# Kernel tuning notes

Hardware: AMD Instinct MI355X
Metric: run time of the kernel (lower is better)

Reference implementation:

```python
import jax, jax.numpy as jnp
import numpy as np
from jax import lax

CW = 8       # current_window
PW = 8       # pretrain_window
HEADS = 8
LOG100 = float(np.log(100.0))


def setup_inputs() -> dict:
    key = jax.random.key(0)
    ks = jax.random.split(key, 8)
    B, H, W, C = 8, 126, 126, 256
    f32 = jnp.float32
    return {
        "x": jax.random.normal(ks[0], (B, H, W, C), f32),
        "w_qkv": jax.random.normal(ks[1], (C, 3 * C), f32) * 0.02,      # 1x1 conv, no bias
        "w_dw": jax.random.normal(ks[2], (3, 3, 1, 3 * C), f32) * 0.1,  # depthwise 3x3, HWIO
        "ln_gamma": jnp.ones((3 * C,), f32),
        "ln_beta": jnp.zeros((3 * C,), f32),
        "q_bias": jnp.zeros((C,), f32),
        "v_bias": jnp.zeros((C,), f32),
        "scale": jnp.full((HEADS, 1, 1), np.log(10.0), f32),
        "cpb_w0": jax.random.normal(ks[3], (2, 512), f32) * 0.02,
        "cpb_b0": jnp.zeros((512,), f32),
        "cpb_w1": jax.random.normal(ks[4], (512, HEADS), f32) * 0.02,   # no bias, sigmoid
        "w_proj": jax.random.normal(ks[5], (C, C), f32) * 0.02,
    }


def _l2n(t):
    # tf.math.l2_normalize with epsilon=1.55e-5
    return t * lax.rsqrt(jnp.maximum(jnp.sum(t * t, axis=-1, keepdims=True), 1.55e-5))


def _cpb_bias(cpb_w0, cpb_b0, cpb_w1, cw, L, heads):
    # log-spaced continuous relative position table (static)
    rel = np.arange(1 - cw, cw, dtype=np.float32)
    rel = np.stack(np.meshgrid(rel, rel, indexing='ij'), axis=-1)  # [2cw-1, 2cw-1, 2]
    rel = rel * (8.0 / (PW - 1.0))
    rel = np.sign(rel) * np.log1p(np.abs(rel)) / np.log(8.0)
    ri = np.arange(cw)
    ri = np.stack(np.meshgrid(ri, ri, indexing='ij'), axis=0).reshape(2, -1)
    ri = ri[:, :, None] - ri[:, None, :] + (cw - 1)
    relidx = (ri[0] * (2 * cw - 1) + ri[1]).reshape(-1)  # [L*L]
    h = jax.nn.relu(jnp.asarray(rel.reshape(-1, 2)) @ cpb_w0 + cpb_b0)
    bias = jax.nn.sigmoid(h @ cpb_w1) * 16.0             # [(2cw-1)^2, heads]
    bias = bias[jnp.asarray(relidx)].reshape(L, L, heads)
    return bias.transpose(2, 0, 1)                        # [heads, L, L]


def reference(x, w_qkv, w_dw, ln_gamma, ln_beta, q_bias, v_bias, scale,
              cpb_w0, cpb_b0, cpb_w1, w_proj):
    B, H, W, C = x.shape
    cw, heads = CW, HEADS
    hd = C // heads
    L = cw * cw

    # qkv 1x1 conv + depthwise 3x3 + layernorm (ConvNorm)
    qkv = jnp.einsum('bhwc,cd->bhwd', x, w_qkv)           # [B,H,W,3C]
    qkv = lax.conv_general_dilated(qkv, w_dw, (1, 1), 'SAME',
                                   dimension_numbers=('NHWC', 'HWIO', 'NHWC'),
                                   feature_group_count=3 * C)
    mu = jnp.mean(qkv, axis=-1, keepdims=True)
    var = jnp.mean(jnp.square(qkv - mu), axis=-1, keepdims=True)
    qkv = (qkv - mu) * lax.rsqrt(var + 1e-5) * ln_gamma + ln_beta
    qkv = qkv + jnp.concatenate([q_bias, jnp.zeros_like(q_bias), v_bias])

    # pad to multiple of window, grid-partition (MaxViT-style strided grid)
    pad_h, pad_w = (-H) % cw, (-W) % cw
    hb, wb = pad_h // 2, pad_w // 2
    qkv = jnp.pad(qkv, ((0, 0), (hb, pad_h - hb), (wb, pad_w - wb), (0, 0)))
    Hp, Wp = H + pad_h, W + pad_w
    Hb, Wb = Hp // cw, Wp // cw
    nw = Hb * Wb
    qkv = qkv.reshape(B, cw, Hb, cw, Wb, 3, heads, hd)
    qkv = qkv.transpose(0, 2, 4, 6, 1, 3, 5, 7).reshape(B * nw, heads, L, 3, hd)
    q, k, v = qkv[..., 0, :], qkv[..., 1, :], qkv[..., 2, :]

    # cosine attention with learned per-head log-scale (clamped at log 100)
    q, k = _l2n(q), _l2n(k)
    ls = jnp.exp(jnp.minimum(scale, LOG100))              # [heads,1,1]
    attn = jnp.einsum('nhqd,nhkd->nhqk', q * ls, k)

    attn = attn + _cpb_bias(cpb_w0, cpb_b0, cpb_w1, cw, L, heads)[None]

    if pad_h + pad_w > 0:
        m = jnp.pad(jnp.ones((1, H, W, 1), attn.dtype),
                    ((0, 0), (hb, pad_h - hb), (wb, pad_w - wb), (0, 0)))
        m = m.reshape(1, cw, Hb, cw, Wb, 1).transpose(0, 2, 4, 1, 3, 5).reshape(nw, L)
        mbias = -100.0 * (m == 0).astype(attn.dtype)       # [nw, L] over keys
        attn = attn.reshape(B, nw, heads, L, L) + mbias[None, :, None, None, :]
        attn = attn.reshape(B * nw, heads, L, L)

    attn = jax.nn.softmax(attn, axis=-1)
    out = jnp.einsum('nhqk,nhkd->nhqd', attn, v)           # [B*nw, heads, L, hd]

    # reverse grid partition + crop + projection
    out = out.reshape(B, Hb, Wb, heads, cw, cw, hd)
    out = out.transpose(0, 4, 1, 5, 2, 3, 6).reshape(B, Hp, Wp, C)
    out = out[:, hb:hb + H, wb:wb + W]
    return jnp.einsum('bhwc,cd->bhwd', out, w_proj)
```

## Files before the change

### kernel.cpp

```cpp
#include <hip/hip_runtime.h>

typedef unsigned short ushort;
typedef __bf16 bf16x8 __attribute__((ext_vector_type(8)));
typedef float f32x4 __attribute__((ext_vector_type(4)));
typedef float f4 __attribute__((ext_vector_type(4)));
typedef unsigned short us8 __attribute__((ext_vector_type(8)));
typedef unsigned short us4 __attribute__((ext_vector_type(4)));
typedef unsigned u32x4v __attribute__((ext_vector_type(4)));

#define NPIX 127008
#define HDIM 126
#define WDIM 126

__device__ __forceinline__ float bf2f(ushort u) {
  unsigned v = ((unsigned)u) << 16;
  return __builtin_bit_cast(float, v);
}
__device__ __forceinline__ ushort f2bf(float f) {
  unsigned x = __builtin_bit_cast(unsigned, f);
  x += 0x7fffu + ((x >> 16) & 1u);
  return (ushort)(x >> 16);
}

__global__ void k_cvt_x(const float* __restrict__ x, ushort* __restrict__ xb, int n8) {
  const int stride = gridDim.x * blockDim.x;
  for (int i = blockIdx.x * blockDim.x + threadIdx.x; i < n8; i += stride) {
    const f4 a = *(const f4*)&x[(size_t)i * 8];
    const f4 b = *(const f4*)&x[(size_t)i * 8 + 4];
    us8 o;
#pragma unroll
    for (int j = 0; j < 4; ++j) { o[j] = f2bf(a[j]); o[4 + j] = f2bf(b[j]); }
    *(us8*)&xb[(size_t)i * 8] = o;
  }
}

__global__ void k_cvt_wT(const float* __restrict__ in, ushort* __restrict__ out, int N, int K) {
  const int t = blockIdx.x * 256 + threadIdx.x;
  const int n = t / K, k = t - n * K;
  out[t] = f2bf(in[(size_t)k * N + n]);
}

__device__ __forceinline__ float frel(int i) {
  const float v = (float)(i - 7) * (8.0f / 7.0f);
  const float a = log1pf(fabsf(v)) * 0.4808983469629878f;
  return v < 0.f ? -a : a;
}

__global__ __launch_bounds__(256) void k_cpb1(const float* __restrict__ w0,
    const float* __restrict__ b0, const float* __restrict__ w1, float* __restrict__ tmp) {
  const int p = blockIdx.x * 4 + (threadIdx.x >> 6);
  const int lane = threadIdx.x & 63;
  if (p >= 225) return;
  const float r0 = frel(p / 15), r1 = frel(p % 15);
  float hv[8];
#pragma unroll
  for (int jj = 0; jj < 8; ++jj) {
    const int j = lane * 8 + jj;
    hv[jj] = fmaxf(0.f, r0 * w0[j] + r1 * w0[512 + j] + b0[j]);
  }
  for (int h = 0; h < 8; ++h) {
    float part = 0.f;
#pragma unroll
    for (int jj = 0; jj < 8; ++jj) part += hv[jj] * w1[(lane * 8 + jj) * 8 + h];
    for (int o = 32; o; o >>= 1) part += __shfl_xor(part, o);
    if (lane == 0) tmp[p * 8 + h] = 16.f / (1.f + __expf(-part));
  }
}

__global__ void k_cpb2(const float* __restrict__ tmp, float* __restrict__ biasV) {
  const int t = blockIdx.x * 256 + threadIdx.x;
  const int h = t >> 12, rest = t & 4095;
  const int ki = rest >> 10, g = (rest >> 8) & 3, q = (rest >> 2) & 63, r = rest & 3;
  const int key = ki * 16 + g * 4 + r;
  const int d0 = (q >> 3) - (key >> 3) + 7, d1 = (q & 7) - (key & 7) + 7;
  biasV[t] = tmp[(d0 * 15 + d1) * 8 + h];
}

#define GLL(g, l) __builtin_amdgcn_global_load_lds( \
    (const __attribute__((address_space(1))) void*)(g), \
    (__attribute__((address_space(3))) void*)(l), 16, 0, 0)

template <int OUTF, int NX>
__global__ __launch_bounds__(256) void k_gemm(const ushort* __restrict__ A,
                                              const ushort* __restrict__ Bt,
                                              void* __restrict__ Cv, int M, int N) {
  constexpr int K = 256;
  __shared__ ushort lsA[128 * 32];
  __shared__ ushort lsB[128 * 32];
  const int tid = threadIdx.x;
  const int wid = tid >> 6, lane = tid & 63;

  const int nwg = gridDim.x;
  const int q8 = nwg >> 3, r8 = nwg & 7;
  const int xcd = blockIdx.x & 7, pos = blockIdx.x >> 3;
  const int lin = (xcd < r8) ? xcd * (q8 + 1) + pos
                             : r8 * (q8 + 1) + (xcd - r8) * q8 + pos;
  const int m0 = (lin / NX) * 128, n0 = (lin % NX) * 128;

  f32x4 acc[4][4];
#pragma unroll
  for (int i = 0; i < 4; ++i)
#pragma unroll
    for (int j = 0; j < 4; ++j) acc[i][j] = 0.f;

  const int srow = tid >> 2, sk = (tid & 3) * 8;
  const int aw = (wid >> 1) * 64, bw = (wid & 1) * 64;
  const int fr = lane & 15, kg = (lane >> 4) * 8;
  char* lA = (char*)lsA + wid * 1024;
  char* lB = (char*)lsB + wid * 1024;

  int ra0 = m0 + srow;      if (ra0 >= M) ra0 = M - 1;
  int ra1 = m0 + srow + 64; if (ra1 >= M) ra1 = M - 1;
  const int rb0 = n0 + srow, rb1 = n0 + srow + 64;

  for (int kt = 0; kt < K; kt += 32) {
    __syncthreads();
    GLL(A + (size_t)ra0 * K + kt + sk, lA);
    GLL(A + (size_t)ra1 * K + kt + sk, lA + 4096);
    GLL(Bt + (size_t)rb0 * K + kt + sk, lB);
    GLL(Bt + (size_t)rb1 * K + kt + sk, lB + 4096);
    __syncthreads();
    bf16x8 af[4], bb[4];
#pragma unroll
    for (int i = 0; i < 4; ++i)
      af[i] = *(const bf16x8*)&lsA[(aw + i * 16 + fr) * 32 + kg];
#pragma unroll
    for (int j = 0; j < 4; ++j)
      bb[j] = *(const bf16x8*)&lsB[(bw + j * 16 + fr) * 32 + kg];
#pragma unroll
    for (int i = 0; i < 4; ++i)
#pragma unroll
      for (int j = 0; j < 4; ++j)
        acc[i][j] = __builtin_amdgcn_mfma_f32_16x16x32_bf16(af[i], bb[j], acc[i][j], 0, 0, 0);
  }

  const int r4 = (lane >> 4) * 4, cc = lane & 15;
#pragma unroll
  for (int i = 0; i < 4; ++i) {
#pragma unroll
    for (int j = 0; j < 4; ++j) {
      const int gc = n0 + bw + j * 16 + cc;
#pragma unroll
      for (int r = 0; r < 4; ++r) {
        const int gr = m0 + aw + i * 16 + r4 + r;
        if (gr < M) {
          if constexpr (OUTF == 0)
            ((ushort*)Cv)[(size_t)gr * N + gc] = f2bf(acc[i][j][r]);
          else
            ((float*)Cv)[(size_t)gr * N + gc] = acc[i][j][r];
        }
      }
    }
  }
}

__global__ __launch_bounds__(192) void k_convln(const ushort* __restrict__ pre,
    const float* __restrict__ wdw,
    const float* __restrict__ gamma, const float* __restrict__ beta,
    const float* __restrict__ qb, const float* __restrict__ vb,
    const float* __restrict__ scale, ushort* __restrict__ qkvw) {
  __shared__ float red[3][2];
  const int nwg = gridDim.x;
  const int q8 = nwg >> 3, r8 = nwg & 7;
  const int xcd = blockIdx.x & 7, pos = blockIdx.x >> 3;
  const int lin = (xcd < r8) ? xcd * (q8 + 1) + pos
                             : r8 * (q8 + 1) + (xcd - r8) * q8 + pos;
  const int rowid = lin % 1008;
  const int seg = lin / 1008;
  const int b = rowid / HDIM, h = rowid - b * HDIM;
  const int chunk = threadIdx.x;
  const int wid = chunk >> 6, lane = chunk & 63;
  const int c0 = chunk * 4;

  float wt[9][4];
#pragma unroll
  for (int tap = 0; tap < 9; ++tap) {
    const f4 wa = *(const f4*)&wdw[tap * 768 + c0];
#pragma unroll
    for (int j = 0; j < 4; ++j) wt[tap][j] = wa[j];
  }
  if (h == 0) {
#pragma unroll
    for (int tap = 0; tap < 3; ++tap)
#pragma unroll
      for (int j = 0; j < 4; ++j) wt[tap][j] = 0.f;
  }
  if (h == HDIM - 1) {
#pragma unroll
    for (int tap = 6; tap < 9; ++tap)
#pragma unroll
      for (int j = 0; j < 4; ++j) wt[tap][j] = 0.f;
  }

  const f4 g4 = *(const f4*)&gamma[c0];
  const f4 b4 = *(const f4*)&beta[c0];
  f4 addb = {0.f, 0.f, 0.f, 0.f};
  if (wid == 0) addb = *(const f4*)&qb[c0];
  if (wid == 2) addb = *(const f4*)&vb[c0 - 512];
  const float ls = (wid == 0) ? __expf(fminf(scale[chunk >> 3], 4.60517025f)) : 1.f;

  const int hm = h > 0 ? h - 1 : 0, hp2 = h < HDIM - 1 ? h + 1 : HDIM - 1;
  const ushort* r0 = pre + (size_t)((b * HDIM + hm) * WDIM) * 768 + c0;
  const ushort* r1 = pre + (size_t)((b * HDIM + h) * WDIM) * 768 + c0;
  const ushort* r2 = pre + (size_t)((b * HDIM + hp2) * WDIM) * 768 + c0;

  const int w0 = seg * 18;
  float b0_[3][4], b1_[3][4], b2_[3][4], b3_[3][4];

#define LOADCOL(dst, w)                                                   \
  {                                                                       \
    us4 u0 = *(const us4*)&r0[(size_t)(w) * 768];                         \
    us4 u1 = *(const us4*)&r1[(size_t)(w) * 768];                         \
    us4 u2 = *(const us4*)&r2[(size_t)(w) * 768];                         \
    _Pragma("unroll") for (int j = 0; j < 4; ++j) {                       \
      dst[0][j] = bf2f(u0[j]); dst[1][j] = bf2f(u1[j]); dst[2][j] = bf2f(u2[j]); } \
  }
#define ZEROCOL(dst)                                                      \
  { _Pragma("unroll") for (int rr = 0; rr < 3; ++rr)                      \
    _Pragma("unroll") for (int j = 0; j < 4; ++j) dst[rr][j] = 0.f; }

  if (w0 > 0) { LOADCOL(b0_, w0 - 1) } else { ZEROCOL(b0_) }
  LOADCOL(b1_, w0)
  LOADCOL(b2_, w0 + 1)

  const int dstc = ((b << 8) + (((h + 1) & 15) << 4)) << 6;
  const int dsth = ((h + 1) >> 4) << 3;

#define BODY(L, C, R, P, w)                                               \
  {                                                                       \
    if ((w) + 2 < WDIM) { LOADCOL(P, (w) + 2) } else { ZEROCOL(P) }       \
    float acc[4];                                                         \
    _Pragma("unroll") for (int j = 0; j < 4; ++j)                         \
      acc[j] = L[0][j] * wt[0][j] + C[0][j] * wt[1][j] + R[0][j] * wt[2][j] \
             + L[1][j] * wt[3][j] + C[1][j] * wt[4][j] + R[1][j] * wt[5][j] \
             + L[2][j] * wt[6][j] + C[2][j] * wt[7][j] + R[2][j] * wt[8][j]; \
            \
    float s_ = acc[0] + acc[1] + acc[2] + acc[3];                         \
    float ss_ = acc[0]*acc[0] + acc[1]*acc[1] + acc[2]*acc[2] + acc[3]*acc[3]; \
    _Pragma("unroll") for (int o = 32; o; o >>= 1) {                      \
      s_ += __shfl_xor(s_, o); ss_ += __shfl_xor(ss_, o); }               \
    if (lane == 0) { red[wid][0] = s_; red[wid][1] = ss_; }               \
    __syncthreads();                                                      \
    const float tot = red[0][0] + red[1][0] + red[2][0];                  \
    const float tot2 = red[0][1] + red[1][1] + red[2][1];                 \
    __syncthreads();                                                      \
    const float mu = tot * (1.f / 768.f);                                 \
    const float var = tot2 * (1.f / 768.f) - mu * mu;                     \
    const float rs = rsqrtf(var + 1e-5f);                                 \
    float y[4];                                                           \
    _Pragma("unroll") for (int j = 0; j < 4; ++j)                         \
      y[j] = (acc[j] - mu) * rs * g4[j] + b4[j] + addb[j];                \
    if (wid < 2) {      \
      float gg = y[0]*y[0] + y[1]*y[1] + y[2]*y[2] + y[3]*y[3];           \
      gg += __shfl_xor(gg, 1); gg += __shfl_xor(gg, 2); gg += __shfl_xor(gg, 4); \
      const float rn = rsqrtf(fmaxf(gg, 1.55e-5f)) * ls;                  \
      _Pragma("unroll") for (int j = 0; j < 4; ++j) y[j] *= rn;           \
    }                                                                     \
    const int wp = (w) + 1;                                               \
    const int dstrow = dstc + ((wp & 15) << 6) + dsth + (wp >> 4);        \
    us4 o;                                                                \
    _Pragma("unroll") for (int j = 0; j < 4; ++j) o[j] = f2bf(y[j]);      \
    *(us4*)&qkvw[(size_t)dstrow * 768 + c0] = o;                          \
  }

#pragma unroll 1
  for (int w = w0; w < w0 + 16; w += 4) {
    BODY(b0_, b1_, b2_, b3_, w)
    BODY(b1_, b2_, b3_, b0_, w + 1)
    BODY(b2_, b3_, b0_, b1_, w + 2)
    BODY(b3_, b0_, b1_, b2_, w + 3)
  }
  BODY(b0_, b1_, b2_, b3_, w0 + 16)
  BODY(b1_, b2_, b3_, b0_, w0 + 17)
#undef BODY
#undef LOADCOL
#undef ZEROCOL
}

__global__ __launch_bounds__(256) void k_attn(const ushort* __restrict__ qkvw,
    const float* __restrict__ biasV, ushort* __restrict__ aout) {
  __shared__ ushort Vs[4][64][36];
  const int wid = threadIdx.x >> 6, lane = threadIdx.x & 63;
  const int u = blockIdx.x * 4 + wid;
  const int head = u >> 11, wl = u & 2047;
  const int b = wl >> 8, wh = (wl >> 4) & 15, ww = wl & 15;
  const int c = lane & 15, g = lane >> 4;
  const int g4 = g * 4, g8 = g * 8;
  const ushort* wb = qkvw + (size_t)wl * 64 * 768;
  const us8 zz = 0;

  const bool e_r0 = (wh == 0), e_r7 = (wh == 15), e_c0 = (ww == 0), e_c7 = (ww == 15);
#define TOKVALID(t) (!(((e_r0) & (((t) >> 3) == 0)) | ((e_r7) & (((t) >> 3) == 7)) | \
                       ((e_c0) & (((t) & 7) == 0)) | ((e_c7) & (((t) & 7) == 7))))

  {
    const bool tv = TOKVALID(lane);
    const ushort* vp = wb + (size_t)lane * 768 + 512 + head * 32;
    us8 v0 = *(const us8*)vp;
    us8 v1 = *(const us8*)(vp + 8);
    us8 v2 = *(const us8*)(vp + 16);
    us8 v3 = *(const us8*)(vp + 24);
    v0 = tv ? v0 : zz;
    v1 = tv ? v1 : zz;
    v2 = tv ? v2 : zz;
    v3 = tv ? v3 : zz;
    ushort* vr = &Vs[wid][lane][0];
    *(us4*)&vr[0]  = __builtin_shufflevector(v0, v0, 0, 1, 2, 3);
    *(us4*)&vr[4]  = __builtin_shufflevector(v0, v0, 4, 5, 6, 7);
    *(us4*)&vr[8]  = __builtin_shufflevector(v1, v1, 0, 1, 2, 3);
    *(us4*)&vr[12] = __builtin_shufflevector(v1, v1, 4, 5, 6, 7);
    *(us4*)&vr[16] = __builtin_shufflevector(v2, v2, 0, 1, 2, 3);
    *(us4*)&vr[20] = __builtin_shufflevector(v2, v2, 4, 5, 6, 7);
    *(us4*)&vr[24] = __builtin_shufflevector(v3, v3, 0, 1, 2, 3);
    *(us4*)&vr[28] = __builtin_shufflevector(v3, v3, 4, 5, 6, 7);
  }

  bf16x8 kf[4], qf[4];
#pragma unroll
  for (int ki = 0; ki < 4; ++ki) {
    const int tk = ki * 16 + c;
    us8 kv = *(const us8*)&wb[(size_t)tk * 768 + 256 + head * 32 + g8];
    kv = TOKVALID(tk) ? kv : zz;
    kf[ki] = __builtin_bit_cast(bf16x8, kv);
  }
#pragma unroll
  for (int qj = 0; qj < 4; ++qj) {
    const int tq = qj * 16 + c;
    us8 qv = *(const us8*)&wb[(size_t)tq * 768 + head * 32 + g8];
    qv = TOKVALID(tq) ? qv : zz;
    qf[qj] = __builtin_bit_cast(bf16x8, qv);
  }

  const float* bvh = biasV + (head << 12);
  f32x4 st[4][4];
#pragma unroll
  for (int ki = 0; ki < 4; ++ki)
#pragma unroll
    for (int qj = 0; qj < 4; ++qj) {
      const f32x4 bfrag = *(const f32x4*)&bvh[((ki * 4 + g) << 8) + ((qj * 16 + c) << 2)];
      st[ki][qj] = __builtin_amdgcn_mfma_f32_16x16x32_bf16(kf[ki], qf[qj], bfrag, 0, 0, 0);
    }

  unsigned afr[4][2][4];
#pragma unroll
  for (int qj = 0; qj < 4; ++qj) {
    float s[16];
#pragma unroll
    for (int ki = 0; ki < 4; ++ki)
#pragma unroll
      for (int r = 0; r < 4; ++r) {
        const int key = ki * 16 + g4 + r;
        s[ki * 4 + r] = TOKVALID(key) ? st[ki][qj][r] : -1e30f;
      }
    float m = s[0];
#pragma unroll
    for (int i = 1; i < 16; ++i) m = fmaxf(m, s[i]);
    m = fmaxf(m, __shfl_xor(m, 16));
    m = fmaxf(m, __shfl_xor(m, 32));
    float den = 0.f;
#pragma unroll
    for (int i = 0; i < 16; ++i) { s[i] = __expf(s[i] - m); den += s[i]; }
    den += __shfl_xor(den, 16);
    den += __shfl_xor(den, 32);
    const float inv = 1.f / den;

    unsigned pk[4][2];
#pragma unroll
    for (int ki = 0; ki < 4; ++ki) {
      pk[ki][0] = ((unsigned)f2bf(s[ki * 4 + 1] * inv) << 16) | f2bf(s[ki * 4 + 0] * inv);
      pk[ki][1] = ((unsigned)f2bf(s[ki * 4 + 3] * inv) << 16) | f2bf(s[ki * 4 + 2] * inv);
    }
#pragma unroll
    for (int j2 = 0; j2 < 4; ++j2) {
      const int src = c + 16 * (2 * (g & 1) + (j2 >> 1));
      const unsigned s0 = __shfl(pk[0][j2 & 1], src);
      const unsigned s1 = __shfl(pk[1][j2 & 1], src);
      const unsigned s2 = __shfl(pk[2][j2 & 1], src);
      const unsigned s3 = __shfl(pk[3][j2 & 1], src);
      afr[qj][0][j2] = (g < 2) ? s0 : s1;
      afr[qj][1][j2] = (g < 2) ? s2 : s3;
    }
  }

  f32x4 ao[4][2];
#pragma unroll
  for (int qi = 0; qi < 4; ++qi)
#pragma unroll
    for (int di = 0; di < 2; ++di) ao[qi][di] = 0.f;
#pragma unroll
  for (int kc = 0; kc < 2; ++kc) {
#pragma unroll
    for (int di = 0; di < 2; ++di) {
      us8 bv;
#pragma unroll
      for (int j = 0; j < 8; ++j) bv[j] = Vs[wid][kc * 32 + g8 + j][di * 16 + c];
      const bf16x8 bb = __builtin_bit_cast(bf16x8, bv);
#pragma unroll
      for (int qi = 0; qi < 4; ++qi) {
        const u32x4v aw4 = {afr[qi][kc][0], afr[qi][kc][1], afr[qi][kc][2], afr[qi][kc][3]};
        ao[qi][di] = __builtin_amdgcn_mfma_f32_16x16x32_bf16(
            __builtin_bit_cast(bf16x8, aw4), bb, ao[qi][di], 0, 0, 0);
      }
    }
  }

#pragma unroll
  for (int qi = 0; qi < 4; ++qi)
#pragma unroll
    for (int r = 0; r < 4; ++r) {
      const int q = qi * 16 + g4 + r;
      if (TOKVALID(q)) {
        const int h = (q >> 3) * 16 + wh - 1, w2 = (q & 7) * 16 + ww - 1;
        ushort* op = aout + ((size_t)((b * HDIM + h) * WDIM + w2)) * 256 + head * 32;
        op[c] = f2bf(ao[qi][0][r]);
        op[16 + c] = f2bf(ao[qi][1][r]);
      }
    }
#undef TOKVALID
}

extern "C" void kernel_launch(void* const* d_in, const int* in_sizes, int n_in,
                              void* d_out, int out_size, void* d_ws, size_t ws_size,
                              hipStream_t stream) {
  (void)in_sizes; (void)n_in; (void)out_size; (void)ws_size;
  const float* x      = (const float*)d_in[0];
  const float* w_qkv  = (const float*)d_in[1];
  const float* w_dw   = (const float*)d_in[2];
  const float* ln_g   = (const float*)d_in[3];
  const float* ln_b   = (const float*)d_in[4];
  const float* q_bias = (const float*)d_in[5];
  const float* v_bias = (const float*)d_in[6];
  const float* scale  = (const float*)d_in[7];
  const float* cpb_w0 = (const float*)d_in[8];
  const float* cpb_b0 = (const float*)d_in[9];
  const float* cpb_w1 = (const float*)d_in[10];
  const float* w_proj = (const float*)d_in[11];
  float* out = (float*)d_out;

  char* ws = (char*)d_ws;
  const size_t PRE  = (size_t)NPIX * 768 * 2;
  const size_t QKVW = (size_t)131072 * 768 * 2;
  ushort* pre    = (ushort*)ws;
  ushort* qkvw   = (ushort*)(ws + PRE);
  ushort* xb     = (ushort*)(ws + PRE);
  ushort* aoutb  = pre;
  ushort* wqkvT  = (ushort*)(ws + PRE + QKVW);
  ushort* wprojT = (ushort*)(ws + PRE + QKVW + (size_t)768 * 256 * 2);
  float*  cpbtmp = (float*)(ws + PRE + QKVW + (size_t)768 * 256 * 2 + (size_t)256 * 256 * 2);
  float*  biasV  = (float*)(ws + PRE + QKVW + (size_t)768 * 256 * 2 + (size_t)256 * 256 * 2 + 8192);

  k_cvt_wT<<<768, 256, 0, stream>>>(w_qkv, wqkvT, 768, 256);
  k_cvt_wT<<<256, 256, 0, stream>>>(w_proj, wprojT, 256, 256);
  k_cpb1<<<57, 256, 0, stream>>>(cpb_w0, cpb_b0, cpb_w1, cpbtmp);
  k_cpb2<<<128, 256, 0, stream>>>(cpbtmp, biasV);
  k_cvt_x<<<2048, 256, 0, stream>>>(x, xb, NPIX * 256 / 8);
  k_gemm<0, 6><<<5958, 256, 0, stream>>>(xb, wqkvT, pre, NPIX, 768);
  k_convln<<<7056, 192, 0, stream>>>(pre, w_dw, ln_g, ln_b, q_bias, v_bias, scale, qkvw);
  k_attn<<<4096, 256, 0, stream>>>(qkvw, biasV, aoutb);
  k_gemm<1, 2><<<1986, 256, 0, stream>>>(aoutb, wprojT, out, NPIX, 256);
}
```

Before: 488.3 us.

## Process two columns per LayerNorm reduction and double-buffer shared partials

Result: no change. 483.9 us (-0.9%).

```diff
diff --git a/kernel.cpp b/kernel.cpp
--- a/kernel.cpp
+++ b/kernel.cpp
@@ -159,7 +159,7 @@
     const float* __restrict__ gamma, const float* __restrict__ beta,
     const float* __restrict__ qb, const float* __restrict__ vb,
     const float* __restrict__ scale, ushort* __restrict__ qkvw) {
-  __shared__ float red[3][2];
+  __shared__ __align__(16) float red[2][3][4];
   const int nwg = gridDim.x;
   const int q8 = nwg >> 3, r8 = nwg & 7;
   const int xcd = blockIdx.x & 7, pos = blockIdx.x >> 3;
@@ -205,7 +205,7 @@
   const ushort* r2 = pre + (size_t)((b * HDIM + hp2) * WDIM) * 768 + c0;
 
   const int w0 = seg * 18;
-  float b0_[3][4], b1_[3][4], b2_[3][4], b3_[3][4];
+  float n0[3][4], n1[3][4], n2[3][4], n3[3][4], n4[3][4], n5[3][4];
 
 #define LOADCOL(dst, w)                                                   \
   {                                                                       \
@@ -219,33 +219,18 @@
   { _Pragma("unroll") for (int rr = 0; rr < 3; ++rr)                      \
     _Pragma("unroll") for (int j = 0; j < 4; ++j) dst[rr][j] = 0.f; }
 
-  if (w0 > 0) { LOADCOL(b0_, w0 - 1) } else { ZEROCOL(b0_) }
-  LOADCOL(b1_, w0)
-  LOADCOL(b2_, w0 + 1)
+  if (w0 > 0) { LOADCOL(n0, w0 - 1) } else { ZEROCOL(n0) }
+  LOADCOL(n1, w0)
+  LOADCOL(n2, w0 + 1)
+  LOADCOL(n3, w0 + 2)
 
   const int dstc = ((b << 8) + (((h + 1) & 15) << 4)) << 6;
   const int dsth = ((h + 1) >> 4) << 3;
 
-#define BODY(L, C, R, P, w)                                               \
+#define EPI(acc, tS, tQ, wp_)                                             \
   {                                                                       \
-    if ((w) + 2 < WDIM) { LOADCOL(P, (w) + 2) } else { ZEROCOL(P) }       \
-    float acc[4];                                                         \
-    _Pragma("unroll") for (int j = 0; j < 4; ++j)                         \
-      acc[j] = L[0][j] * wt[0][j] + C[0][j] * wt[1][j] + R[0][j] * wt[2][j] \
-             + L[1][j] * wt[3][j] + C[1][j] * wt[4][j] + R[1][j] * wt[5][j] \
-             + L[2][j] * wt[6][j] + C[2][j] * wt[7][j] + R[2][j] * wt[8][j]; \
-            \
-    float s_ = acc[0] + acc[1] + acc[2] + acc[3];                         \
-    float ss_ = acc[0]*acc[0] + acc[1]*acc[1] + acc[2]*acc[2] + acc[3]*acc[3]; \
-    _Pragma("unroll") for (int o = 32; o; o >>= 1) {                      \
-      s_ += __shfl_xor(s_, o); ss_ += __shfl_xor(ss_, o); }               \
-    if (lane == 0) { red[wid][0] = s_; red[wid][1] = ss_; }               \
-    __syncthreads();                                                      \
-    const float tot = red[0][0] + red[1][0] + red[2][0];                  \
-    const float tot2 = red[0][1] + red[1][1] + red[2][1];                 \
-    __syncthreads();                                                      \
-    const float mu = tot * (1.f / 768.f);                                 \
-    const float var = tot2 * (1.f / 768.f) - mu * mu;                     \
+    const float mu = (tS) * (1.f / 768.f);                                \
+    const float var = (tQ) * (1.f / 768.f) - mu * mu;                     \
     const float rs = rsqrtf(var + 1e-5f);                                 \
     float y[4];                                                           \
     _Pragma("unroll") for (int j = 0; j < 4; ++j)                         \
@@ -256,23 +241,51 @@
       const float rn = rsqrtf(fmaxf(gg, 1.55e-5f)) * ls;                  \
       _Pragma("unroll") for (int j = 0; j < 4; ++j) y[j] *= rn;           \
     }                                                                     \
-    const int wp = (w) + 1;                                               \
-    const int dstrow = dstc + ((wp & 15) << 6) + dsth + (wp >> 4);        \
+    const int dstrow = dstc + (((wp_) & 15) << 6) + dsth + ((wp_) >> 4);  \
     us4 o;                                                                \
     _Pragma("unroll") for (int j = 0; j < 4; ++j) o[j] = f2bf(y[j]);      \
     *(us4*)&qkvw[(size_t)dstrow * 768 + c0] = o;                          \
   }
 
+#define PHASE(A, B, C, D, E, F, w)                                        \
+  {                                                                       \
+    if ((w) + 3 < WDIM) { LOADCOL(E, (w) + 3) } else { ZEROCOL(E) }       \
+    if ((w) + 4 < WDIM) { LOADCOL(F, (w) + 4) } else { ZEROCOL(F) }       \
+    float a0[4], a1[4];                                                   \
+    _Pragma("unroll") for (int j = 0; j < 4; ++j) {                       \
+      a0[j] = A[0][j]*wt[0][j] + B[0][j]*wt[1][j] + C[0][j]*wt[2][j]      \
+            + A[1][j]*wt[3][j] + B[1][j]*wt[4][j] + C[1][j]*wt[5][j]      \
+            + A[2][j]*wt[6][j] + B[2][j]*wt[7][j] + C[2][j]*wt[8][j];     \
+      a1[j] = B[0][j]*wt[0][j] + C[0][j]*wt[1][j] + D[0][j]*wt[2][j]      \
+            + B[1][j]*wt[3][j] + C[1][j]*wt[4][j] + D[1][j]*wt[5][j]      \
+            + B[2][j]*wt[6][j] + C[2][j]*wt[7][j] + D[2][j]*wt[8][j];     \
+    }                                                                     \
+    float s0 = a0[0]+a0[1]+a0[2]+a0[3];                                   \
+    float p0 = a0[0]*a0[0]+a0[1]*a0[1]+a0[2]*a0[2]+a0[3]*a0[3];           \
+    float s1 = a1[0]+a1[1]+a1[2]+a1[3];                                   \
+    float p1 = a1[0]*a1[0]+a1[1]*a1[1]+a1[2]*a1[2]+a1[3]*a1[3];           \
+    _Pragma("unroll") for (int o = 32; o; o >>= 1) {                      \
+      s0 += __shfl_xor(s0, o); p0 += __shfl_xor(p0, o);                   \
+      s1 += __shfl_xor(s1, o); p1 += __shfl_xor(p1, o); }                 \
+    const int par = ((w) >> 1) & 1;                                       \
+    if (lane == 0) { f4 rv = {s0, p0, s1, p1}; *(f4*)&red[par][wid][0] = rv; } \
+    __syncthreads();                                                      \
+    const float t0 = red[par][0][0] + red[par][1][0] + red[par][2][0];    \
+    const float u0_ = red[par][0][1] + red[par][1][1] + red[par][2][1];   \
+    const float t1 = red[par][0][2] + red[par][1][2] + red[par][2][2];    \
+    const float u1_ = red[par][0][3] + red[par][1][3] + red[par][2][3];   \
+    EPI(a0, t0, u0_, (w) + 1)                                             \
+    EPI(a1, t1, u1_, (w) + 2)                                             \
+  }
+
 #pragma unroll 1
-  for (int w = w0; w < w0 + 16; w += 4) {
-    BODY(b0_, b1_, b2_, b3_, w)
-    BODY(b1_, b2_, b3_, b0_, w + 1)
-    BODY(b2_, b3_, b0_, b1_, w + 2)
-    BODY(b3_, b0_, b1_, b2_, w + 3)
-  }
-  BODY(b0_, b1_, b2_, b3_, w0 + 16)
-  BODY(b1_, b2_, b3_, b0_, w0 + 17)
-#undef BODY
+  for (int w = w0; w < w0 + 18; w += 6) {
+    PHASE(n0, n1, n2, n3, n4, n5, w)
+    PHASE(n2, n3, n4, n5, n0, n1, w + 2)
+    PHASE(n4, n5, n0, n1, n2, n3, w + 4)
+  }
+#undef PHASE
+#undef EPI
 #undef LOADCOL
 #undef ZEROCOL
 }
```
